# Optimization experiments

Hardware: AMD Instinct MI355X
Metric: run time of the kernel (lower is better)

Reference implementation:

```python
import jax, jax.numpy as jnp
import numpy as np

B, S, D = 2, 2048, 1024
H = 16            # attention heads
KVH = 4           # key/value heads
G = H // KVH      # group_size = 4
HD = D // H       # head_dim = 64
ROPE_THETA = 10000.0


def rope(x):
    # x: [B, S, D]; interleaved-pair rotary embedding over full last dim
    d = x.shape[-1]
    inv_freq = 1.0 / (ROPE_THETA ** (jnp.arange(0, d, 2, dtype=jnp.float32) / d))  # [d/2]
    ang = jnp.arange(x.shape[1], dtype=jnp.float32)[:, None] * inv_freq[None, :]   # [S, d/2]
    cos, sin = jnp.cos(ang), jnp.sin(ang)
    x1, x2 = x[..., 0::2], x[..., 1::2]
    r1 = x1 * cos - x2 * sin
    r2 = x1 * sin + x2 * cos
    out = jnp.stack([r1, r2], axis=-1).reshape(x.shape)
    return out


def setup_inputs() -> dict:
    key = jax.random.key(0)
    kx, kq, kk, kv = jax.random.split(key, 4)
    x = jax.random.normal(kx, (B, S, D), dtype=jnp.float32)
    # mark last 256 positions of batch element 1 as padding via NaN
    x = x.at[1, S - 256:, :].set(jnp.nan)
    scale = 1.0 / np.sqrt(D)
    Wq = jax.random.normal(kq, (D, D), dtype=jnp.float32) * scale
    Wk = jax.random.normal(kk, (D, D // G), dtype=jnp.float32) * scale
    Wv = jax.random.normal(kv, (D, D // G), dtype=jnp.float32) * scale
    return {"x": x, "Wq": Wq, "Wk": Wk, "Wv": Wv}


def reference(x, Wq, Wk, Wv):
    pad = jnp.isnan(x)                      # [B,S,D]
    x = jnp.where(pad, 0.0, x)
    key_pad = jnp.any(pad, axis=-1)         # [B,S] True = padded token

    q = x @ Wq                              # [B,S,D]
    k = jnp.repeat(x @ Wk, G, axis=-1)      # grouped KV, repeat_interleave -> [B,S,D]
    v = jnp.repeat(x @ Wv, G, axis=-1)

    q = rope(q)
    k = rope(k)

    def split_heads(t):
        return t.reshape(B, S, H, HD).transpose(0, 2, 1, 3)  # [B,H,S,HD]

    q, k, v = split_heads(q), split_heads(k), split_heads(v)

    scores = jnp.einsum('bhqd,bhkd->bhqk', q, k) / np.sqrt(HD)
    causal = jnp.tril(jnp.ones((S, S), dtype=bool))
    allow = causal[None, None, :, :] & (~key_pad)[:, None, None, :]
    scores = jnp.where(allow, scores, -1e9)
    attn = jax.nn.softmax(scores, axis=-1)
    out = jnp.einsum('bhqk,bhkd->bhqd', attn, v)
    return out.transpose(0, 2, 1, 3).reshape(B, S, D)
```

## Files before the change

### kernel.cpp

```cpp
#include <hip/hip_runtime.h>
#include <hip/hip_bf16.h>
#include <math.h>

typedef unsigned short u16;
typedef unsigned int u32;
typedef __bf16 bf16x8 __attribute__((ext_vector_type(8)));
typedef short s16x4 __attribute__((ext_vector_type(4)));
typedef float fx4 __attribute__((ext_vector_type(4)));

#define MFMA16(a, b, c) __builtin_amdgcn_mfma_f32_16x16x32_bf16(a, b, c, 0, 0, 0)
#define MFMAPV(a, b, c) __builtin_amdgcn_mfma_f32_16x16x16bf16_1k(a, b, c, 0, 0, 0)

static constexpr int Bb = 2, Ss = 2048, Dd = 1024, Hh = 16, DKV = 256;
static constexpr int ROWS = Bb * Ss;
static constexpr float L2T_OVER = 0.0259525632f;
static constexpr float SC2 = 0.18033688f;

__device__ __forceinline__ u16 f2bf(float f) {
    union { float f; u32 i; } v; v.f = f;
    u32 u = v.i;
    return (u16)((u + 0x7FFFu + ((u >> 16) & 1u)) >> 16);
}
__device__ __forceinline__ u32 f2bfu(float f) {
    u32 u = __float_as_uint(f);
    return (u + 0x7FFFu + ((u >> 16) & 1u)) >> 16;
}

__device__ __forceinline__ float fexp2(float x) {
    float r; asm("v_exp_f32 %0, %1" : "=v"(r) : "v"(x)); return r;
}
__device__ __forceinline__ void fsincos(float a, float& sn, float& cs) {
    float r = a * 0.15915494309189535f;
    r = r - floorf(r);
    asm("v_sin_f32 %0, %1" : "=v"(sn) : "v"(r));
    asm("v_cos_f32 %0, %1" : "=v"(cs) : "v"(r));
}

__device__ __forceinline__ void gl16(const u16* g, u16* l) {
    __builtin_amdgcn_global_load_lds(
        (const __attribute__((address_space(1))) void*)g,
        (__attribute__((address_space(3))) void*)l, 16, 0, 0);
}

template <int CTRL>
__device__ __forceinline__ float dppf(float x) {
    return __int_as_float(
        __builtin_amdgcn_mov_dpp(__float_as_int(x), CTRL, 0xF, 0xF, true));
}

__global__ void pre_kernel(const float* __restrict__ x, const float* __restrict__ Wq,
                           const float* __restrict__ Wk, const float* __restrict__ Wv,
                           u16* __restrict__ xc, u32* __restrict__ kpb,
                           u16* __restrict__ wAll) {
    __shared__ u16 tile[32][33];
    __shared__ int flag;
    int bid = blockIdx.x, t = threadIdx.x;
    if (bid < 4096) {
        int row = bid;
        if (t == 0) flag = 0;
        __syncthreads();
        float4 d = *(const float4*)(x + (size_t)row * Dd + t * 4);
        int any = 0;
        float a0 = d.x, a1 = d.y, a2 = d.z, a3 = d.w;
        if ((__float_as_uint(a0) & 0x7FFFFFFFu) > 0x7F800000u) { a0 = 0.f; any = 1; }
        if ((__float_as_uint(a1) & 0x7FFFFFFFu) > 0x7F800000u) { a1 = 0.f; any = 1; }
        if ((__float_as_uint(a2) & 0x7FFFFFFFu) > 0x7F800000u) { a2 = 0.f; any = 1; }
        if ((__float_as_uint(a3) & 0x7FFFFFFFu) > 0x7F800000u) { a3 = 0.f; any = 1; }
        if (any) atomicOr(&flag, 1);
        uint2 o;
        o.x = (u32)f2bf(a0) | ((u32)f2bf(a1) << 16);
        o.y = (u32)f2bf(a2) | ((u32)f2bf(a3) << 16);
        *(uint2*)(xc + (size_t)row * Dd + t * 4) = o;
        __syncthreads();
        if (t == 0 && flag) {
            int b = row >> 11, s = row & (Ss - 1);
            atomicOr(&kpb[b * 64 + (s >> 5)], 1u << (s & 31));
        }
        return;
    }
    const float* in; u16* out; int C, bx, by;
    if (bid < 5120) { int i = bid - 4096; in = Wq; out = wAll; C = Dd; bx = i & 31; by = i >> 5; }
    else if (bid < 5376) { int i = bid - 5120; in = Wk; out = wAll + (size_t)Dd * Dd; C = DKV; bx = i & 7; by = i >> 3; }
    else { int i = bid - 5376; in = Wv; out = wAll + (size_t)1280 * Dd; C = DKV; bx = i & 7; by = i >> 3; }
    int c0 = bx * 32, r0 = by * 32;
    int tx = t & 31, ty = t >> 5;
    for (int i = 0; i < 32; i += 8)
        tile[ty + i][tx] = f2bf(in[(size_t)(r0 + ty + i) * C + c0 + tx]);
    __syncthreads();
    for (int i = 0; i < 32; i += 8)
        out[(size_t)(c0 + ty + i) * Dd + r0 + tx] = tile[tx][ty + i];
}

__global__ __launch_bounds__(256) void gemm_qkv(
    const u16* __restrict__ A, const u16* __restrict__ Bt, u16* __restrict__ qbuf,
    u16* __restrict__ kr, u16* __restrict__ vtb) {
    __shared__ __align__(16) u16 As[2][128 * 32];
    __shared__ __align__(16) u16 Bs[2][64 * 32];
    int t = threadIdx.x, w = t >> 6, lane = t & 63;
    int l15 = lane & 15, quad = lane >> 4;
    int col0 = blockIdx.x * 64, row0 = blockIdx.y * 128;
    int wm = w >> 1, wn = w & 1;
    fx4 acc[4][2];
#pragma unroll
    for (int i = 0; i < 4; ++i)
#pragma unroll
        for (int j = 0; j < 2; ++j) acc[i][j] = (fx4){0.f, 0.f, 0.f, 0.f};

    auto stage = [&](int kb, int buf) {
#pragma unroll
        for (int i = 0; i < 2; ++i) {
            int slot = i * 256 + t;
            int row = slot >> 2, p = slot & 3, g = p ^ ((row >> 1) & 3);
            gl16(A + (size_t)(row0 + row) * Dd + kb * 32 + g * 8,
                 &As[buf][(i * 256 + w * 64) * 8]);
        }
        {
            int row = t >> 2, p = t & 3, g = p ^ ((row >> 1) & 3);
            gl16(Bt + (size_t)(col0 + row) * Dd + kb * 32 + g * 8,
                 &Bs[buf][(w * 64) * 8]);
        }
    };

    stage(0, 0);
    int buf = 0;
    for (int kb = 0; kb < 32; ++kb) {
        __syncthreads();
        if (kb + 1 < 32) stage(kb + 1, buf ^ 1);
        bf16x8 af[4], bf[2];
#pragma unroll
        for (int mi = 0; mi < 4; ++mi) {
            int row = wm * 64 + mi * 16 + l15;
            af[mi] = *(const bf16x8*)(&As[buf][row * 32 + ((quad ^ ((row >> 1) & 3)) * 8)]);
        }
#pragma unroll
        for (int ni = 0; ni < 2; ++ni) {
            int row = wn * 32 + ni * 16 + l15;
            bf[ni] = *(const bf16x8*)(&Bs[buf][row * 32 + ((quad ^ ((row >> 1) & 3)) * 8)]);
        }
#pragma unroll
        for (int mi = 0; mi < 4; ++mi)
#pragma unroll
            for (int ni = 0; ni < 2; ++ni)
                acc[mi][ni] = MFMA16(af[mi], bf[ni], acc[mi][ni]);
        buf ^= 1;
    }

    if (col0 < 1024) {
        bool oddc = (l15 & 1) != 0;
#pragma unroll
        for (int mi = 0; mi < 4; ++mi) {
            int rbase = row0 + wm * 64 + mi * 16 + quad * 4;
#pragma unroll
            for (int ni = 0; ni < 2; ++ni) {
                int ccol = col0 + wn * 32 + ni * 16 + l15;
                float f = fexp2(-(float)(ccol >> 1) * L2T_OVER);
#pragma unroll
                for (int r = 0; r < 4; ++r) {
                    float v = acc[mi][ni][r];
                    float p = dppf<0xB1>(v);
                    float x0 = oddc ? p : v, x1 = oddc ? v : p;
                    float pos = (float)((rbase + r) & (Ss - 1));
                    float sn, cs;
                    fsincos(pos * f, sn, cs);
                    float res = oddc ? (x0 * sn + x1 * cs) : (x0 * cs - x1 * sn);
                    qbuf[(size_t)(rbase + r) * Dd + ccol] = f2bf(res);
                }
            }
        }
    } else if (col0 < 1280) {
#pragma unroll
        for (int mi = 0; mi < 4; ++mi) {
            int rbase = row0 + wm * 64 + mi * 16 + quad * 4;
#pragma unroll
            for (int ni = 0; ni < 2; ++ni) {
                int tt = col0 + wn * 32 + ni * 16 + l15 - 1024;
                float f0 = fexp2(-(float)(2 * tt) * L2T_OVER);
                float f1 = fexp2(-(float)(2 * tt + 1) * L2T_OVER);
#pragma unroll
                for (int r = 0; r < 4; ++r) {
                    int row = rbase + r;
                    float pos = (float)(row & (Ss - 1));
                    float s0, c0, s1, c1;
                    fsincos(pos * f0, s0, c0);
                    fsincos(pos * f1, s1, c1);
                    float kv = acc[mi][ni][r];
                    uint2 o;
                    o.x = (u32)f2bf(kv * (c0 - s0)) | ((u32)f2bf(kv * (s0 + c0)) << 16);
                    o.y = (u32)f2bf(kv * (c1 - s1)) | ((u32)f2bf(kv * (s1 + c1)) << 16);
                    *(uint2*)(kr + (size_t)row * Dd + 4 * tt) = o;
                }
            }
        }
    } else {
#pragma unroll
        for (int mi = 0; mi < 4; ++mi) {
            int rbase = row0 + wm * 64 + mi * 16 + quad * 4;
            int b = rbase >> 11, s0 = rbase & (Ss - 1);
#pragma unroll
            for (int ni = 0; ni < 2; ++ni) {
                int c = col0 + wn * 32 + ni * 16 + l15 - 1280;
                uint2 o;
                o.x = (u32)f2bf(acc[mi][ni][0]) | ((u32)f2bf(acc[mi][ni][1]) << 16);
                o.y = (u32)f2bf(acc[mi][ni][2]) | ((u32)f2bf(acc[mi][ni][3]) << 16);
                *(uint2*)(vtb + (size_t)(b * DKV + c) * Ss + s0) = o;
            }
        }
    }
}

__global__ __launch_bounds__(256) void attn_kernel(
    const u16* __restrict__ qbuf, const u16* __restrict__ kr,
    const u16* __restrict__ vt, const u32* __restrict__ kpb,
    float* __restrict__ O4, float* __restrict__ L4) {
    __shared__ __align__(16) u16 Ks[2][64 * 64];

    int t = threadIdx.x, w = t >> 6, lane = t & 63;
    int l15 = lane & 15, quad = lane >> 4;
    int bid = blockIdx.x;
    int u = bid >> 5, hh = bid & 31;
    int tile, c;
    if (u < 32)      { tile = 24 + (u & 7); c = u >> 3; }
    else if (u < 56) { tile = 16 + ((u - 32) & 7); c = (u - 32) >> 3; }
    else if (u < 72) { tile = 8 + ((u - 56) & 7); c = (u - 56) >> 3; }
    else             { tile = u - 72; c = 0; }
    int b = hh >> 4, h = hh & 15;
    int n = tile + 1, C = (n + 7) >> 3;
    int kb0 = (int)((u32)(n * c) / (u32)C);
    int kbe = (int)((u32)(n * (c + 1)) / (u32)C);
    int q0 = tile * 64;

    int qq = q0 + w * 16 + l15;
    const u16* qp = qbuf + (size_t)(b * Ss + qq) * Dd + h * 64;
    bf16x8 qf0 = *(const bf16x8*)(qp + quad * 8);
    bf16x8 qf1 = *(const bf16x8*)(qp + 32 + quad * 8);

    u32 pw_all = kpb[b * 64 + lane];

    const u16* vrow = vt + (size_t)(b * DKV + h * 16 + l15) * Ss;

    auto stageK = [&](int k0, int buf) {
#pragma unroll
        for (int i2 = 0; i2 < 2; ++i2) {
            int row = i2 * 32 + w * 8 + (lane >> 3);
            int gg = (lane & 7) ^ (row & 7);
            gl16(kr + (size_t)(b * Ss + k0 + row) * Dd + h * 64 + gg * 8,
                 &Ks[buf][(i2 * 32 + w * 8) * 64]);
        }
    };

    float l_lane = 0.f;
    fx4 oacc = (fx4){0.f, 0.f, 0.f, 0.f};

    stageK(kb0 * 64, 0);
    int buf = 0;
    const int qmin = q0 + w * 16;
    const int kk = quad * 4;

    for (int kb = kb0; kb < kbe; ++kb) {
        int k0 = kb * 64;
        __syncthreads();
        if (kb + 1 < kbe) stageK(k0 + 64, buf ^ 1);

        s16x4 vf[4];
#pragma unroll
        for (int tt = 0; tt < 4; ++tt)
            vf[tt] = *(const s16x4*)(vrow + k0 + tt * 16 + kk);

        fx4 s[4];
#pragma unroll
        for (int tt = 0; tt < 4; ++tt) {
            const u16* kb_ = &Ks[buf][(tt * 16 + l15) * 64];
            bf16x8 kf0 = *(const bf16x8*)(kb_ + ((quad ^ (l15 & 7)) * 8));
            bf16x8 kf1 = *(const bf16x8*)(kb_ + (((quad + 4) ^ (l15 & 7)) * 8));
            fx4 z = (fx4){0.f, 0.f, 0.f, 0.f};
            fx4 a = MFMA16(kf0, qf0, z);
            s[tt] = MFMA16(kf1, qf1, a);
        }

        u32 pw0 = (u32)__shfl((int)pw_all, 2 * kb, 64);
        u32 pw1 = (u32)__shfl((int)pw_all, 2 * kb + 1, 64);
        bool fast = (k0 + 63 <= qmin) & ((pw0 | pw1) == 0u);

        float e[4][4];
        if (fast) {
#pragma unroll
            for (int tt = 0; tt < 4; ++tt)
#pragma unroll
                for (int r = 0; r < 4; ++r)
                    e[tt][r] = fexp2(fmaf(s[tt][r], SC2, -32.f));
        } else {
#pragma unroll
            for (int tt = 0; tt < 4; ++tt) {
                u32 bits = ((tt & 2) ? pw1 : pw0) >> ((tt * 16 + kk) & 31);
                int kbase = k0 + tt * 16 + kk;
#pragma unroll
                for (int r = 0; r < 4; ++r) {
                    float ee = fexp2(fmaf(s[tt][r], SC2, -32.f));
                    e[tt][r] = (kbase + r <= qq && !((bits >> r) & 1u)) ? ee : 0.f;
                }
            }
        }

#pragma unroll
        for (int tt = 0; tt < 4; ++tt) {
            l_lane += (e[tt][0] + e[tt][1]) + (e[tt][2] + e[tt][3]);
            union { u32 uu[2]; s16x4 v; } pk;
            pk.uu[0] = f2bfu(e[tt][0]) | (f2bfu(e[tt][1]) << 16);
            pk.uu[1] = f2bfu(e[tt][2]) | (f2bfu(e[tt][3]) << 16);
            oacc = MFMAPV(vf[tt], pk.v, oacc);
        }
        buf ^= 1;
    }

    float l_red = l_lane;
    l_red += __shfl_xor(l_red, 16, 64);
    l_red += __shfl_xor(l_red, 32, 64);
    size_t slot = ((size_t)hh * Ss + qq) * 4 + c;
    *(fx4*)(&O4[slot * 16 + kk]) = oacc;
    if (lane < 16) L4[slot] = l_red;
}

__global__ void norm_kernel(const float* __restrict__ O4, const float* __restrict__ L4,
                            float* __restrict__ out) {
    int idx = blockIdx.x * 256 + threadIdx.x;
    int d4 = idx & 255;
    int row = idx >> 8;
    int h = d4 >> 4, f = d4 & 15;
    int b = row >> 11, s = row & (Ss - 1);
    int hh = b * 16 + h;
    int Cn = ((s >> 6) + 8) >> 3;
    size_t base = ((size_t)hh * Ss + s) * 4;
    float o = 0.f, l = 0.f;
    for (int c = 0; c < Cn; ++c) {
        o += O4[(base + c) * 16 + f];
        l += L4[base + c];
    }
    float a = o / l;
    float4 o4 = {a, a, a, a};
    *(float4*)(out + (size_t)row * Dd + d4 * 4) = o4;
}

extern "C" void kernel_launch(void* const* d_in, const int* in_sizes, int n_in,
                              void* d_out, int out_size, void* d_ws, size_t ws_size,
                              hipStream_t stream) {
    const float* x = (const float*)d_in[0];
    const float* Wq = (const float*)d_in[1];
    const float* Wk = (const float*)d_in[2];
    const float* Wv = (const float*)d_in[3];
    float* out = (float*)d_out;

    char* ws = (char*)d_ws;
    const size_t SZ_XC = (size_t)ROWS * Dd * 2;
    const size_t SZ_WALL = (size_t)1536 * Dd * 2;
    const size_t SZ_QB = (size_t)ROWS * Dd * 2;
    const size_t SZ_KR = (size_t)ROWS * Dd * 2;
    const size_t SZ_VTB = (size_t)Bb * DKV * Ss * 2;
    const size_t SZ_KPB = 4096;
    const size_t SZ_O4 = (size_t)32 * Ss * 4 * 16 * 4;
    const size_t SZ_L4 = (size_t)32 * Ss * 4 * 4;

    size_t off = 0;
    u16* xc = (u16*)(ws + off); off += SZ_XC;
    u16* wAll = (u16*)(ws + off); off += SZ_WALL;
    u16* qbuf = (u16*)(ws + off); off += SZ_QB;
    u16* kr = (u16*)(ws + off); off += SZ_KR;
    u16* vtb = (u16*)(ws + off); off += SZ_VTB;
    u32* kpb = (u32*)(ws + off); off += SZ_KPB;
    float* O4 = (float*)(ws + off); off += SZ_O4;
    float* L4 = (float*)(ws + off); off += SZ_L4;
    (void)ws_size; (void)in_sizes; (void)n_in; (void)out_size;

    hipMemsetAsync(kpb, 0, SZ_KPB, stream);
    pre_kernel<<<5632, 256, 0, stream>>>(x, Wq, Wk, Wv, xc, kpb, wAll);
    gemm_qkv<<<dim3(1536 / 64, ROWS / 128), 256, 0, stream>>>(xc, wAll, qbuf, kr, vtb);
    attn_kernel<<<2560, 256, 0, stream>>>(qbuf, kr, vtb, kpb, O4, L4);
    norm_kernel<<<4096, 256, 0, stream>>>(O4, L4, out);
}
```

Before: 159.0 us.

## Split attention key range across waves with private K buffers and LDS reduction

Each wave now owns all 64 query rows of the tile and processes its own slice of 32-key sub-blocks, with a private double-buffered K staging area. This replaces the block-wide __syncthreads per key block with a per-wave vmcnt wait. At the end the four waves' partial outputs and row sums are combined through shared memory. The cost is more registers (four Q fragments and four accumulators per wave), plus a launch-bounds occupancy hint and a final reduction step.

Measured after the change: 149.3 us. 6.1% less time.

```diff
diff --git a/kernel.cpp b/kernel.cpp
--- a/kernel.cpp
+++ b/kernel.cpp
@@ -208,11 +208,11 @@
     }
 }
 
-__global__ __launch_bounds__(256) void attn_kernel(
+__global__ __launch_bounds__(256, 4) void attn_kernel(
     const u16* __restrict__ qbuf, const u16* __restrict__ kr,
     const u16* __restrict__ vt, const u32* __restrict__ kpb,
     float* __restrict__ O4, float* __restrict__ L4) {
-    __shared__ __align__(16) u16 Ks[2][64 * 64];
+    __shared__ __align__(16) u16 KsAll[4][2][32 * 64];
 
     int t = threadIdx.x, w = t >> 6, lane = t & 63;
     int l15 = lane & 15, quad = lane >> 4;
@@ -229,95 +229,108 @@
     int kbe = (int)((u32)(n * (c + 1)) / (u32)C);
     int q0 = tile * 64;
 
-    int qq = q0 + w * 16 + l15;
-    const u16* qp = qbuf + (size_t)(b * Ss + qq) * Dd + h * 64;
-    bf16x8 qf0 = *(const bf16x8*)(qp + quad * 8);
-    bf16x8 qf1 = *(const bf16x8*)(qp + 32 + quad * 8);
+    int ST = (kbe - kb0) * 2;
+    int ws0 = kb0 * 2 + (ST * w) / 4;
+    int ws1 = kb0 * 2 + (ST * (w + 1)) / 4;
+
+    bf16x8 qf0[4], qf1[4];
+#pragma unroll
+    for (int m = 0; m < 4; ++m) {
+        const u16* qp = qbuf + (size_t)(b * Ss + q0 + m * 16 + l15) * Dd + h * 64;
+        qf0[m] = *(const bf16x8*)(qp + quad * 8);
+        qf1[m] = *(const bf16x8*)(qp + 32 + quad * 8);
+    }
 
     u32 pw_all = kpb[b * 64 + lane];
-
     const u16* vrow = vt + (size_t)(b * DKV + h * 16 + l15) * Ss;
-
-    auto stageK = [&](int k0, int buf) {
-#pragma unroll
-        for (int i2 = 0; i2 < 2; ++i2) {
-            int row = i2 * 32 + w * 8 + (lane >> 3);
+    u16* myK = &KsAll[w][0][0];
+
+    auto stageK = [&](int sb, int bu) {
+#pragma unroll
+        for (int i2 = 0; i2 < 4; ++i2) {
+            int row = i2 * 8 + (lane >> 3);
             int gg = (lane & 7) ^ (row & 7);
-            gl16(kr + (size_t)(b * Ss + k0 + row) * Dd + h * 64 + gg * 8,
-                 &Ks[buf][(i2 * 32 + w * 8) * 64]);
+            gl16(kr + (size_t)(b * Ss + sb * 32 + row) * Dd + h * 64 + gg * 8,
+                 myK + bu * 2048 + i2 * 512);
         }
     };
 
-    float l_lane = 0.f;
-    fx4 oacc = (fx4){0.f, 0.f, 0.f, 0.f};
-
-    stageK(kb0 * 64, 0);
+    float l_lane[4] = {0.f, 0.f, 0.f, 0.f};
+    fx4 oacc[4];
+#pragma unroll
+    for (int m = 0; m < 4; ++m) oacc[m] = (fx4){0.f, 0.f, 0.f, 0.f};
+
+    if (ws0 < ws1) stageK(ws0, 0);
     int buf = 0;
-    const int qmin = q0 + w * 16;
     const int kk = quad * 4;
 
-    for (int kb = kb0; kb < kbe; ++kb) {
-        int k0 = kb * 64;
-        __syncthreads();
-        if (kb + 1 < kbe) stageK(k0 + 64, buf ^ 1);
-
-        s16x4 vf[4];
-#pragma unroll
-        for (int tt = 0; tt < 4; ++tt)
-            vf[tt] = *(const s16x4*)(vrow + k0 + tt * 16 + kk);
-
-        fx4 s[4];
-#pragma unroll
-        for (int tt = 0; tt < 4; ++tt) {
-            const u16* kb_ = &Ks[buf][(tt * 16 + l15) * 64];
+    for (int sb = ws0; sb < ws1; ++sb) {
+        asm volatile("s_waitcnt vmcnt(0)" ::: "memory");
+        __builtin_amdgcn_sched_barrier(0);
+        if (sb + 1 < ws1) stageK(sb + 1, buf ^ 1);
+        int k0 = sb * 32;
+        u32 pw = (u32)__shfl((int)pw_all, sb, 64);
+
+#pragma unroll
+        for (int tt = 0; tt < 2; ++tt) {
+            const u16* kb_ = myK + buf * 2048 + (tt * 16 + l15) * 64;
             bf16x8 kf0 = *(const bf16x8*)(kb_ + ((quad ^ (l15 & 7)) * 8));
             bf16x8 kf1 = *(const bf16x8*)(kb_ + (((quad + 4) ^ (l15 & 7)) * 8));
-            fx4 z = (fx4){0.f, 0.f, 0.f, 0.f};
-            fx4 a = MFMA16(kf0, qf0, z);
-            s[tt] = MFMA16(kf1, qf1, a);
-        }
-
-        u32 pw0 = (u32)__shfl((int)pw_all, 2 * kb, 64);
-        u32 pw1 = (u32)__shfl((int)pw_all, 2 * kb + 1, 64);
-        bool fast = (k0 + 63 <= qmin) & ((pw0 | pw1) == 0u);
-
-        float e[4][4];
-        if (fast) {
-#pragma unroll
-            for (int tt = 0; tt < 4; ++tt)
-#pragma unroll
-                for (int r = 0; r < 4; ++r)
-                    e[tt][r] = fexp2(fmaf(s[tt][r], SC2, -32.f));
-        } else {
-#pragma unroll
-            for (int tt = 0; tt < 4; ++tt) {
-                u32 bits = ((tt & 2) ? pw1 : pw0) >> ((tt * 16 + kk) & 31);
-                int kbase = k0 + tt * 16 + kk;
-#pragma unroll
-                for (int r = 0; r < 4; ++r) {
-                    float ee = fexp2(fmaf(s[tt][r], SC2, -32.f));
-                    e[tt][r] = (kbase + r <= qq && !((bits >> r) & 1u)) ? ee : 0.f;
+            s16x4 vf = *(const s16x4*)(vrow + k0 + tt * 16 + kk);
+            int kbase = k0 + tt * 16 + kk;
+            u32 bits = pw >> (tt * 16 + kk);
+#pragma unroll
+            for (int m = 0; m < 4; ++m) {
+                fx4 z = (fx4){0.f, 0.f, 0.f, 0.f};
+                fx4 a = MFMA16(kf0, qf0[m], z);
+                fx4 s = MFMA16(kf1, qf1[m], a);
+                float e[4];
+                if ((k0 + 31 <= q0 + m * 16) & (pw == 0u)) {
+#pragma unroll
+                    for (int r = 0; r < 4; ++r)
+                        e[r] = fexp2(fmaf(s[r], SC2, -32.f));
+                } else {
+                    int qq = q0 + m * 16 + l15;
+#pragma unroll
+                    for (int r = 0; r < 4; ++r) {
+                        float ee = fexp2(fmaf(s[r], SC2, -32.f));
+                        e[r] = (kbase + r <= qq && !((bits >> r) & 1u)) ? ee : 0.f;
+                    }
                 }
+                l_lane[m] += (e[0] + e[1]) + (e[2] + e[3]);
+                union { u32 uu[2]; s16x4 v; } pk;
+                pk.uu[0] = f2bfu(e[0]) | (f2bfu(e[1]) << 16);
+                pk.uu[1] = f2bfu(e[2]) | (f2bfu(e[3]) << 16);
+                oacc[m] = MFMAPV(vf, pk.v, oacc[m]);
             }
         }
-
-#pragma unroll
-        for (int tt = 0; tt < 4; ++tt) {
-            l_lane += (e[tt][0] + e[tt][1]) + (e[tt][2] + e[tt][3]);
-            union { u32 uu[2]; s16x4 v; } pk;
-            pk.uu[0] = f2bfu(e[tt][0]) | (f2bfu(e[tt][1]) << 16);
-            pk.uu[1] = f2bfu(e[tt][2]) | (f2bfu(e[tt][3]) << 16);
-            oacc = MFMAPV(vf[tt], pk.v, oacc);
-        }
         buf ^= 1;
     }
 
-    float l_red = l_lane;
-    l_red += __shfl_xor(l_red, 16, 64);
-    l_red += __shfl_xor(l_red, 32, 64);
-    size_t slot = ((size_t)hh * Ss + qq) * 4 + c;
-    *(fx4*)(&O4[slot * 16 + kk]) = oacc;
-    if (lane < 16) L4[slot] = l_red;
+    float* fw = (float*)myK;
+#pragma unroll
+    for (int m = 0; m < 4; ++m) {
+        float lr = l_lane[m];
+        lr += __shfl_xor(lr, 16, 64);
+        lr += __shfl_xor(lr, 32, 64);
+        *(fx4*)(fw + (m * 16 + l15) * 16 + kk) = oacc[m];
+        if (quad == 0) fw[1024 + m * 16 + l15] = lr;
+    }
+    __syncthreads();
+
+    int q = t >> 2, f4 = t & 3;
+    fx4 os = (fx4){0.f, 0.f, 0.f, 0.f};
+    float ls = 0.f;
+#pragma unroll
+    for (int wv = 0; wv < 4; ++wv) {
+        const float* fv = (const float*)&KsAll[wv][0][0];
+        fx4 ov = *(const fx4*)(fv + q * 16 + f4 * 4);
+        os[0] += ov[0]; os[1] += ov[1]; os[2] += ov[2]; os[3] += ov[3];
+        if (f4 == 0) ls += fv[1024 + q];
+    }
+    size_t slot = ((size_t)hh * Ss + (q0 + q)) * 4 + c;
+    *(fx4*)(&O4[slot * 16 + f4 * 4]) = os;
+    if (f4 == 0) L4[slot] = ls;
 }
 
 __global__ void norm_kernel(const float* __restrict__ O4, const float* __restrict__ L4,
```
